# Optimization experiments

Measured on AMD Instinct MI355X. Metric: run time of the kernel, lower is better.

## Reference

```python
import jax, jax.numpy as jnp
import numpy as np

N_NODES = 100000
N_EDGES = 3200000
N_IN = 5
N_OUT = 16


def setup_inputs() -> dict:
    key = jax.random.key(0)
    k1, k2, k3, k4 = jax.random.split(key, 4)
    atom = jax.random.normal(k1, (N_NODES, N_IN), dtype=jnp.float32)
    edge_index = jax.random.randint(k2, (2, N_EDGES), 0, N_NODES, dtype=jnp.int64)
    # Linear(n_input=5, n_neural=16) parameters
    W = jax.random.normal(k3, (N_OUT, N_IN), dtype=jnp.float32) / np.sqrt(N_IN)
    b = jax.random.normal(k4, (N_OUT,), dtype=jnp.float32) * 0.01
    return {"atom": atom, "edge_index": edge_index, "W": W, "b": b}


def reference(atom, edge_index, W, b):
    n = atom.shape[0]
    # add_self_loops
    loops = jnp.arange(n, dtype=edge_index.dtype)
    row = jnp.concatenate([edge_index[0], loops])  # source nodes [E+N]
    col = jnp.concatenate([edge_index[1], loops])  # target nodes [E+N]
    # x = Linear(atom)
    x = atom @ W.T + b  # [N, n_out]
    # degree over target index (includes self loops -> deg >= 1)
    deg = jax.ops.segment_sum(jnp.ones_like(col, dtype=x.dtype), col, num_segments=n)
    dis = deg ** -0.5  # deg_inv_sqrt, finite since deg >= 1
    norm = dis[row] * dis[col]  # [E+N]
    # gather-scale-scatter: message = norm * x_j, aggr='add' at col
    msgs = norm[:, None] * x[row]  # [E+N, n_out]
    out = jax.ops.segment_sum(msgs, col, num_segments=n)  # [N, n_out]
    return jax.nn.relu(out)
```

## Files before the change

kernel.cpp:

```cpp
#include <hip/hip_runtime.h>

#define N_IN 5
#define N_OUT 16
#define NB 256
#define BN 400
#define CAP 14336
#define QSCALE 1024.0f
#define QBIAS 8192
#define BIN_MAGIC 10737419ull

__device__ __forceinline__ int bin_of(int c) {
    return (int)(((unsigned long long)(unsigned)c * BIN_MAGIC) >> 32);
}

__global__ void init_kernel(int* __restrict__ cursor) {
    if (threadIdx.x < NB) cursor[threadIdx.x] = threadIdx.x * CAP;
}

__global__ __launch_bounds__(1024) void partition_kernel(
        const int* __restrict__ row, const int* __restrict__ col,
        int e, int* __restrict__ eb, int* __restrict__ cursor) {
    __shared__ int hist[NB];
    __shared__ int base[NB];
    int e4 = e >> 2;
    int nchunk = (e4 + 1023) / 1024;
    const int4* rowv = (const int4*)row;
    const int4* colv = (const int4*)col;
    for (int ch = blockIdx.x; ch < nchunk; ch += gridDim.x) {
        int i = ch * 1024 + threadIdx.x;
        bool valid = i < e4;
        int rr[4], cc[4], bb[4], pr[4];
        if (valid) {
            int4 r4 = rowv[i];
            int4 c4 = colv[i];
            rr[0] = r4.x; rr[1] = r4.y; rr[2] = r4.z; rr[3] = r4.w;
            cc[0] = c4.x; cc[1] = c4.y; cc[2] = c4.z; cc[3] = c4.w;
        }
        if (threadIdx.x < NB) hist[threadIdx.x] = 0;
        __syncthreads();
        if (valid) {
#pragma unroll
            for (int j = 0; j < 4; ++j) {
                bb[j] = bin_of(cc[j]);
                pr[j] = atomicAdd(&hist[bb[j]], 1);
            }
        }
        __syncthreads();
        if (threadIdx.x < NB) {
            int h = hist[threadIdx.x];
            base[threadIdx.x] = h ? atomicAdd(&cursor[threadIdx.x], h) : 0;
        }
        __syncthreads();
        if (valid) {
#pragma unroll
            for (int j = 0; j < 4; ++j) {
                int p = base[bb[j]] + pr[j];
                if (p < (bb[j] + 1) * CAP)
                    eb[p] = ((cc[j] - bb[j] * BN) << 17) | rr[j];
            }
        }
        __syncthreads();
    }
    if (blockIdx.x == 0) {
        for (int i = (e4 << 2) + (int)threadIdx.x; i < e; i += (int)blockDim.x) {
            int c = col[i];
            int b = bin_of(c);
            int p = atomicAdd(&cursor[b], 1);
            if (p < (b + 1) * CAP) eb[p] = ((c - b * BN) << 17) | row[i];
        }
    }
}

__global__ __launch_bounds__(1024) void deg_quant_kernel(
        const int* __restrict__ eb, const int* __restrict__ cursor,
        const float* __restrict__ atom,
        ulonglong2* __restrict__ qdatom, unsigned short* __restrict__ deg16,
        int n) {
    __shared__ int hist[BN];
    int bin = blockIdx.x;
    if (threadIdx.x < BN) hist[threadIdx.x] = 0;
    __syncthreads();
    int s0 = bin * CAP;
    int cnt = min(max(cursor[bin] - s0, 0), CAP);
    const int4* ebv = (const int4*)(eb + s0);
    int cnt4 = cnt >> 2;
    for (int i = threadIdx.x; i < cnt4; i += 1024) {
        int4 v = ebv[i];
        atomicAdd(&hist[v.x >> 17], 1);
        atomicAdd(&hist[v.y >> 17], 1);
        atomicAdd(&hist[v.z >> 17], 1);
        atomicAdd(&hist[v.w >> 17], 1);
    }
    for (int i = (cnt4 << 2) + (int)threadIdx.x; i < cnt; i += 1024)
        atomicAdd(&hist[eb[s0 + i] >> 17], 1);
    __syncthreads();
    int l = threadIdx.x;
    if (l >= BN) return;
    int node = bin * BN + l;
    if (node >= n) return;
    int deg = hist[l];
    deg16[node] = (unsigned short)deg;
    float d = rsqrtf((float)(deg + 1));
    const float* ap = atom + (size_t)node * N_IN;
    unsigned long long f[6];
#pragma unroll
    for (int k = 0; k < 5; ++k) {
        int q = __float2int_rn(d * ap[k] * QSCALE);
        q = min(max(q, -8191), 8191);
        f[k] = (unsigned long long)(q + QBIAS);
    }
    f[5] = (unsigned long long)(__float2int_rn(d * QSCALE) + QBIAS);
    ulonglong2 v;
    v.x = f[0] | (f[1] << 21) | (f[2] << 42);
    v.y = f[3] | (f[4] << 21) | (f[5] << 42);
    qdatom[node] = v;
}

__global__ __launch_bounds__(1024) void accum_final(
        const int* __restrict__ eb, const int* __restrict__ cursor,
        const ulonglong2* __restrict__ qdatom,
        const unsigned short* __restrict__ deg16,
        const float* __restrict__ atom,
        const float* __restrict__ W, const float* __restrict__ bias,
        float* __restrict__ out, int n) {
    __shared__ unsigned long long accA[BN];
    __shared__ unsigned long long accB[BN];
    int bin = blockIdx.x;
    if (threadIdx.x < BN) { accA[threadIdx.x] = 0ull; accB[threadIdx.x] = 0ull; }
    __syncthreads();
    int s0 = bin * CAP;
    int cnt = min(max(cursor[bin] - s0, 0), CAP);
    const int4* ebv = (const int4*)(eb + s0);
    int cnt4 = cnt >> 2;
    for (int i = threadIdx.x; i < cnt4; i += 1024) {
        int4 v = ebv[i];
        ulonglong2 q0 = qdatom[v.x & 0x1FFFF];
        ulonglong2 q1 = qdatom[v.y & 0x1FFFF];
        ulonglong2 q2 = qdatom[v.z & 0x1FFFF];
        ulonglong2 q3 = qdatom[v.w & 0x1FFFF];
        atomicAdd(&accA[v.x >> 17], q0.x);
        atomicAdd(&accB[v.x >> 17], q0.y);
        atomicAdd(&accA[v.y >> 17], q1.x);
        atomicAdd(&accB[v.y >> 17], q1.y);
        atomicAdd(&accA[v.z >> 17], q2.x);
        atomicAdd(&accB[v.z >> 17], q2.y);
        atomicAdd(&accA[v.w >> 17], q3.x);
        atomicAdd(&accB[v.w >> 17], q3.y);
    }
    for (int i = (cnt4 << 2) + (int)threadIdx.x; i < cnt; i += 1024) {
        int v = eb[s0 + i];
        ulonglong2 q = qdatom[v & 0x1FFFF];
        atomicAdd(&accA[v >> 17], q.x);
        atomicAdd(&accB[v >> 17], q.y);
    }
    __syncthreads();
    int l = threadIdx.x;
    if (l >= BN) return;
    int node = bin * BN + l;
    if (node >= n) return;
    unsigned long long SA = accA[l], SB = accB[l];
    int deg = deg16[node];
    int db = deg * QBIAS;
    const float inv = 1.0f / QSCALE;
    float s[6];
    s[0] = (float)((int)((SA      ) & 0x1FFFFF) - db) * inv;
    s[1] = (float)((int)((SA >> 21) & 0x1FFFFF) - db) * inv;
    s[2] = (float)((int)((SA >> 42) & 0x1FFFFF) - db) * inv;
    s[3] = (float)((int)((SB      ) & 0x1FFFFF) - db) * inv;
    s[4] = (float)((int)((SB >> 21) & 0x1FFFFF) - db) * inv;
    s[5] = (float)((int)((SB >> 42) & 0x1FFFFF) - db) * inv;
    float d = rsqrtf((float)(deg + 1));
    const float* ap = atom + (size_t)node * N_IN;
    float t5[5];
#pragma unroll
    for (int k = 0; k < 5; ++k) t5[k] = d * (s[k] + d * ap[k]);
    float t1 = d * (s[5] + d);
    float ov[N_OUT];
#pragma unroll
    for (int o = 0; o < N_OUT; ++o) {
        float a = bias[o] * t1;
#pragma unroll
        for (int k = 0; k < 5; ++k) a = fmaf(W[o * N_IN + k], t5[k], a);
        ov[o] = fmaxf(a, 0.0f);
    }
    float4* op = (float4*)(out + (size_t)node * N_OUT);
#pragma unroll
    for (int q = 0; q < 4; ++q)
        op[q] = make_float4(ov[4 * q], ov[4 * q + 1], ov[4 * q + 2], ov[4 * q + 3]);
}

extern "C" void kernel_launch(void* const* d_in, const int* in_sizes, int n_in,
                              void* d_out, int out_size, void* d_ws, size_t ws_size,
                              hipStream_t stream) {
    const float* atom = (const float*)d_in[0];
    const int*   eidx = (const int*)d_in[1];
    const float* W    = (const float*)d_in[2];
    const float* b    = (const float*)d_in[3];
    float* out = (float*)d_out;

    int n = in_sizes[0] / N_IN;
    int e = in_sizes[1] / 2;
    const int* row = eidx;
    const int* col = eidx + e;

    auto align256 = [](size_t v) { return (v + 255) & ~(size_t)255; };
    char* w = (char*)d_ws;
    int*            cursor = (int*)w;            w += align256(NB * 4);
    int*            eb     = (int*)w;            w += align256((size_t)NB * CAP * 4);
    ulonglong2*     qdatom = (ulonglong2*)w;     w += align256((size_t)NB * BN * 16);
    unsigned short* deg16  = (unsigned short*)w;

    init_kernel<<<1, NB, 0, stream>>>(cursor);
    partition_kernel<<<256, 1024, 0, stream>>>(row, col, e, eb, cursor);
    deg_quant_kernel<<<NB, 1024, 0, stream>>>(eb, cursor, atom, qdatom, deg16, n);
    accum_final<<<NB, 1024, 0, stream>>>(eb, cursor, qdatom, deg16, atom, W, b, out, n);
}
```

Baseline: 126.2 us.

## Fuse degree/quantize and accumulate kernels via cooperative grid sync with register-held edges

Merges the degree-histogram/quantization kernel and the accumulate/finalize kernel into one cooperative kernel. The kernel loads each bin's edges into registers once, builds the degree histogram, writes the quantized scaled features, does a grid-wide sync, then gathers and accumulates from the same registers. This drops the second read of the edge buckets, the deg16 buffer and one launch. The cursor is now a per-bin offset cleared by a memset instead of an init kernel. It depends on cooperative launch with 256 blocks of 1024 threads all being resident, and it holds at most 4096 int4 per bin in registers, which matches CAP.

```diff
diff --git a/kernel.cpp b/kernel.cpp
--- a/kernel.cpp
+++ b/kernel.cpp
@@ -1,4 +1,7 @@
 #include <hip/hip_runtime.h>
+#include <hip/hip_cooperative_groups.h>
+
+namespace cg = cooperative_groups;
 
 #define N_IN 5
 #define N_OUT 16
@@ -11,10 +14,6 @@
 
 __device__ __forceinline__ int bin_of(int c) {
     return (int)(((unsigned long long)(unsigned)c * BIN_MAGIC) >> 32);
-}
-
-__global__ void init_kernel(int* __restrict__ cursor) {
-    if (threadIdx.x < NB) cursor[threadIdx.x] = threadIdx.x * CAP;
 }
 
 __global__ __launch_bounds__(1024) void partition_kernel(
@@ -54,9 +53,9 @@
         if (valid) {
 #pragma unroll
             for (int j = 0; j < 4; ++j) {
-                int p = base[bb[j]] + pr[j];
-                if (p < (bb[j] + 1) * CAP)
-                    eb[p] = ((cc[j] - bb[j] * BN) << 17) | rr[j];
+                int o = base[bb[j]] + pr[j];
+                if (o < CAP)
+                    eb[bb[j] * CAP + o] = ((cc[j] - bb[j] * BN) << 17) | rr[j];
             }
         }
         __syncthreads();
@@ -65,102 +64,104 @@
         for (int i = (e4 << 2) + (int)threadIdx.x; i < e; i += (int)blockDim.x) {
             int c = col[i];
             int b = bin_of(c);
-            int p = atomicAdd(&cursor[b], 1);
-            if (p < (b + 1) * CAP) eb[p] = ((c - b * BN) << 17) | row[i];
-        }
-    }
-}
-
-__global__ __launch_bounds__(1024) void deg_quant_kernel(
+            int o = atomicAdd(&cursor[b], 1);
+            if (o < CAP) eb[b * CAP + o] = ((c - b * BN) << 17) | row[i];
+        }
+    }
+}
+
+__global__ __launch_bounds__(1024) void fused_deg_accum(
         const int* __restrict__ eb, const int* __restrict__ cursor,
         const float* __restrict__ atom,
-        ulonglong2* __restrict__ qdatom, unsigned short* __restrict__ deg16,
-        int n) {
-    __shared__ int hist[BN];
-    int bin = blockIdx.x;
-    if (threadIdx.x < BN) hist[threadIdx.x] = 0;
-    __syncthreads();
-    int s0 = bin * CAP;
-    int cnt = min(max(cursor[bin] - s0, 0), CAP);
-    const int4* ebv = (const int4*)(eb + s0);
-    int cnt4 = cnt >> 2;
-    for (int i = threadIdx.x; i < cnt4; i += 1024) {
-        int4 v = ebv[i];
-        atomicAdd(&hist[v.x >> 17], 1);
-        atomicAdd(&hist[v.y >> 17], 1);
-        atomicAdd(&hist[v.z >> 17], 1);
-        atomicAdd(&hist[v.w >> 17], 1);
-    }
-    for (int i = (cnt4 << 2) + (int)threadIdx.x; i < cnt; i += 1024)
-        atomicAdd(&hist[eb[s0 + i] >> 17], 1);
-    __syncthreads();
-    int l = threadIdx.x;
-    if (l >= BN) return;
-    int node = bin * BN + l;
-    if (node >= n) return;
-    int deg = hist[l];
-    deg16[node] = (unsigned short)deg;
-    float d = rsqrtf((float)(deg + 1));
-    const float* ap = atom + (size_t)node * N_IN;
-    unsigned long long f[6];
-#pragma unroll
-    for (int k = 0; k < 5; ++k) {
-        int q = __float2int_rn(d * ap[k] * QSCALE);
-        q = min(max(q, -8191), 8191);
-        f[k] = (unsigned long long)(q + QBIAS);
-    }
-    f[5] = (unsigned long long)(__float2int_rn(d * QSCALE) + QBIAS);
-    ulonglong2 v;
-    v.x = f[0] | (f[1] << 21) | (f[2] << 42);
-    v.y = f[3] | (f[4] << 21) | (f[5] << 42);
-    qdatom[node] = v;
-}
-
-__global__ __launch_bounds__(1024) void accum_final(
-        const int* __restrict__ eb, const int* __restrict__ cursor,
-        const ulonglong2* __restrict__ qdatom,
-        const unsigned short* __restrict__ deg16,
-        const float* __restrict__ atom,
+        ulonglong2* __restrict__ qdatom,
         const float* __restrict__ W, const float* __restrict__ bias,
         float* __restrict__ out, int n) {
+    __shared__ int hist[BN];
     __shared__ unsigned long long accA[BN];
     __shared__ unsigned long long accB[BN];
-    int bin = blockIdx.x;
-    if (threadIdx.x < BN) { accA[threadIdx.x] = 0ull; accB[threadIdx.x] = 0ull; }
+    cg::grid_group grid = cg::this_grid();
+    const int bin = blockIdx.x;
+    const int tid = threadIdx.x;
+    if (tid < BN) { hist[tid] = 0; accA[tid] = 0ull; accB[tid] = 0ull; }
     __syncthreads();
-    int s0 = bin * CAP;
-    int cnt = min(max(cursor[bin] - s0, 0), CAP);
+
+    const int s0 = bin * CAP;
+    const int cnt = min(max(cursor[bin], 0), CAP);
+    const int cnt4 = cnt >> 2;
     const int4* ebv = (const int4*)(eb + s0);
-    int cnt4 = cnt >> 2;
-    for (int i = threadIdx.x; i < cnt4; i += 1024) {
-        int4 v = ebv[i];
-        ulonglong2 q0 = qdatom[v.x & 0x1FFFF];
-        ulonglong2 q1 = qdatom[v.y & 0x1FFFF];
-        ulonglong2 q2 = qdatom[v.z & 0x1FFFF];
-        ulonglong2 q3 = qdatom[v.w & 0x1FFFF];
-        atomicAdd(&accA[v.x >> 17], q0.x);
-        atomicAdd(&accB[v.x >> 17], q0.y);
-        atomicAdd(&accA[v.y >> 17], q1.x);
-        atomicAdd(&accB[v.y >> 17], q1.y);
-        atomicAdd(&accA[v.z >> 17], q2.x);
-        atomicAdd(&accB[v.z >> 17], q2.y);
-        atomicAdd(&accA[v.w >> 17], q3.x);
-        atomicAdd(&accB[v.w >> 17], q3.y);
-    }
-    for (int i = (cnt4 << 2) + (int)threadIdx.x; i < cnt; i += 1024) {
-        int v = eb[s0 + i];
-        ulonglong2 q = qdatom[v & 0x1FFFF];
-        atomicAdd(&accA[v >> 17], q.x);
-        atomicAdd(&accB[v >> 17], q.y);
-    }
+
+    int4 e0, e1, e2, e3;
+    const bool v0 = tid          < cnt4;
+    const bool v1 = tid + 1024   < cnt4;
+    const bool v2 = tid + 2048   < cnt4;
+    const bool v3 = tid + 3072   < cnt4;
+    if (v0) e0 = ebv[tid];
+    if (v1) e1 = ebv[tid + 1024];
+    if (v2) e2 = ebv[tid + 2048];
+    if (v3) e3 = ebv[tid + 3072];
+    int tl = -1;
+    if (tid < (cnt & 3)) tl = eb[s0 + (cnt4 << 2) + tid];
+
+#define H4(E) { atomicAdd(&hist[(E).x >> 17], 1); atomicAdd(&hist[(E).y >> 17], 1); \
+                atomicAdd(&hist[(E).z >> 17], 1); atomicAdd(&hist[(E).w >> 17], 1); }
+    if (v0) H4(e0);
+    if (v1) H4(e1);
+    if (v2) H4(e2);
+    if (v3) H4(e3);
+#undef H4
+    if (tl >= 0) atomicAdd(&hist[tl >> 17], 1);
     __syncthreads();
-    int l = threadIdx.x;
-    if (l >= BN) return;
-    int node = bin * BN + l;
-    if (node >= n) return;
-    unsigned long long SA = accA[l], SB = accB[l];
-    int deg = deg16[node];
-    int db = deg * QBIAS;
+
+    int mydeg = 0;
+    float a0 = 0.f, a1 = 0.f, a2 = 0.f, a3 = 0.f, a4 = 0.f;
+    const int node = bin * BN + tid;
+    const bool own = (tid < BN) && (node < n);
+    if (own) {
+        mydeg = hist[tid];
+        float d = rsqrtf((float)(mydeg + 1));
+        const float* ap = atom + (size_t)node * N_IN;
+        a0 = ap[0]; a1 = ap[1]; a2 = ap[2]; a3 = ap[3]; a4 = ap[4];
+        unsigned long long f[6];
+        float av[5] = {a0, a1, a2, a3, a4};
+#pragma unroll
+        for (int k = 0; k < 5; ++k) {
+            int q = __float2int_rn(d * av[k] * QSCALE);
+            q = min(max(q, -8191), 8191);
+            f[k] = (unsigned long long)(q + QBIAS);
+        }
+        f[5] = (unsigned long long)(__float2int_rn(d * QSCALE) + QBIAS);
+        ulonglong2 v;
+        v.x = f[0] | (f[1] << 21) | (f[2] << 42);
+        v.y = f[3] | (f[4] << 21) | (f[5] << 42);
+        qdatom[node] = v;
+    }
+    __threadfence();
+    grid.sync();
+
+#define A4(E) { \
+        ulonglong2 q0 = qdatom[(E).x & 0x1FFFF]; \
+        ulonglong2 q1 = qdatom[(E).y & 0x1FFFF]; \
+        ulonglong2 q2 = qdatom[(E).z & 0x1FFFF]; \
+        ulonglong2 q3 = qdatom[(E).w & 0x1FFFF]; \
+        atomicAdd(&accA[(E).x >> 17], q0.x); atomicAdd(&accB[(E).x >> 17], q0.y); \
+        atomicAdd(&accA[(E).y >> 17], q1.x); atomicAdd(&accB[(E).y >> 17], q1.y); \
+        atomicAdd(&accA[(E).z >> 17], q2.x); atomicAdd(&accB[(E).z >> 17], q2.y); \
+        atomicAdd(&accA[(E).w >> 17], q3.x); atomicAdd(&accB[(E).w >> 17], q3.y); }
+    if (v0) A4(e0);
+    if (v1) A4(e1);
+    if (v2) A4(e2);
+    if (v3) A4(e3);
+#undef A4
+    if (tl >= 0) {
+        ulonglong2 q = qdatom[tl & 0x1FFFF];
+        atomicAdd(&accA[tl >> 17], q.x);
+        atomicAdd(&accB[tl >> 17], q.y);
+    }
+    __syncthreads();
+
+    if (!own) return;
+    unsigned long long SA = accA[tid], SB = accB[tid];
+    int db = mydeg * QBIAS;
     const float inv = 1.0f / QSCALE;
     float s[6];
     s[0] = (float)((int)((SA      ) & 0x1FFFFF) - db) * inv;
@@ -169,11 +170,11 @@
     s[3] = (float)((int)((SB      ) & 0x1FFFFF) - db) * inv;
     s[4] = (float)((int)((SB >> 21) & 0x1FFFFF) - db) * inv;
     s[5] = (float)((int)((SB >> 42) & 0x1FFFFF) - db) * inv;
-    float d = rsqrtf((float)(deg + 1));
-    const float* ap = atom + (size_t)node * N_IN;
+    float d = rsqrtf((float)(mydeg + 1));
     float t5[5];
-#pragma unroll
-    for (int k = 0; k < 5; ++k) t5[k] = d * (s[k] + d * ap[k]);
+    float av[5] = {a0, a1, a2, a3, a4};
+#pragma unroll
+    for (int k = 0; k < 5; ++k) t5[k] = d * (s[k] + d * av[k]);
     float t1 = d * (s[5] + d);
     float ov[N_OUT];
 #pragma unroll
@@ -205,13 +206,18 @@
 
     auto align256 = [](size_t v) { return (v + 255) & ~(size_t)255; };
     char* w = (char*)d_ws;
-    int*            cursor = (int*)w;            w += align256(NB * 4);
-    int*            eb     = (int*)w;            w += align256((size_t)NB * CAP * 4);
-    ulonglong2*     qdatom = (ulonglong2*)w;     w += align256((size_t)NB * BN * 16);
-    unsigned short* deg16  = (unsigned short*)w;
-
-    init_kernel<<<1, NB, 0, stream>>>(cursor);
+    int*        cursor = (int*)w;        w += align256(NB * 4);
+    int*        eb     = (int*)w;        w += align256((size_t)NB * CAP * 4);
+    ulonglong2* qdatom = (ulonglong2*)w;
+
+    hipMemsetAsync(cursor, 0, NB * sizeof(int), stream);
     partition_kernel<<<256, 1024, 0, stream>>>(row, col, e, eb, cursor);
-    deg_quant_kernel<<<NB, 1024, 0, stream>>>(eb, cursor, atom, qdatom, deg16, n);
-    accum_final<<<NB, 1024, 0, stream>>>(eb, cursor, qdatom, deg16, atom, W, b, out, n);
-}
+
+    const int* eb_c = eb;
+    const int* cursor_c = cursor;
+    void* kargs[] = { (void*)&eb_c, (void*)&cursor_c, (void*)&atom,
+                      (void*)&qdatom, (void*)&W, (void*)&b,
+                      (void*)&out, (void*)&n };
+    hipLaunchCooperativeKernel((void*)fused_deg_accum, dim3(NB), dim3(1024),
+                               kargs, 0, stream);
+}
```

Measured after the change: 230.3 us. 82.5% more time.

## Compute node degrees with global atomics during partition, drop degree-histogram pass

Applied to the files above, without the earlier changes.

Moves the in-degree count into the partition kernel as per-edge global atomicAdds on a zeroed degree array, so the separate kernel that re-read every bin's edges to histogram degrees is replaced by a light per-node quantization kernel. The init kernel is replaced by a memset that zeroes both the cursors (now relative offsets) and the degree array. This removes one full pass over the 3.2M binned edges but adds 3.2M random global atomics to the partition phase, which may contend or add latency.

```diff
diff --git a/kernel.cpp b/kernel.cpp
--- a/kernel.cpp
+++ b/kernel.cpp
@@ -13,13 +13,10 @@
     return (int)(((unsigned long long)(unsigned)c * BIN_MAGIC) >> 32);
 }
 
-__global__ void init_kernel(int* __restrict__ cursor) {
-    if (threadIdx.x < NB) cursor[threadIdx.x] = threadIdx.x * CAP;
-}
-
 __global__ __launch_bounds__(1024) void partition_kernel(
         const int* __restrict__ row, const int* __restrict__ col,
-        int e, int* __restrict__ eb, int* __restrict__ cursor) {
+        int e, int* __restrict__ eb, int* __restrict__ cursor,
+        int* __restrict__ deg) {
     __shared__ int hist[NB];
     __shared__ int base[NB];
     int e4 = e >> 2;
@@ -43,6 +40,7 @@
             for (int j = 0; j < 4; ++j) {
                 bb[j] = bin_of(cc[j]);
                 pr[j] = atomicAdd(&hist[bb[j]], 1);
+                atomicAdd(&deg[cc[j]], 1);
             }
         }
         __syncthreads();
@@ -54,9 +52,9 @@
         if (valid) {
 #pragma unroll
             for (int j = 0; j < 4; ++j) {
-                int p = base[bb[j]] + pr[j];
-                if (p < (bb[j] + 1) * CAP)
-                    eb[p] = ((cc[j] - bb[j] * BN) << 17) | rr[j];
+                int o = base[bb[j]] + pr[j];
+                if (o < CAP)
+                    eb[bb[j] * CAP + o] = ((cc[j] - bb[j] * BN) << 17) | rr[j];
             }
         }
         __syncthreads();
@@ -65,42 +63,19 @@
         for (int i = (e4 << 2) + (int)threadIdx.x; i < e; i += (int)blockDim.x) {
             int c = col[i];
             int b = bin_of(c);
-            int p = atomicAdd(&cursor[b], 1);
-            if (p < (b + 1) * CAP) eb[p] = ((c - b * BN) << 17) | row[i];
+            int o = atomicAdd(&cursor[b], 1);
+            atomicAdd(&deg[c], 1);
+            if (o < CAP) eb[b * CAP + o] = ((c - b * BN) << 17) | row[i];
         }
     }
 }
 
-__global__ __launch_bounds__(1024) void deg_quant_kernel(
-        const int* __restrict__ eb, const int* __restrict__ cursor,
-        const float* __restrict__ atom,
-        ulonglong2* __restrict__ qdatom, unsigned short* __restrict__ deg16,
-        int n) {
-    __shared__ int hist[BN];
-    int bin = blockIdx.x;
-    if (threadIdx.x < BN) hist[threadIdx.x] = 0;
-    __syncthreads();
-    int s0 = bin * CAP;
-    int cnt = min(max(cursor[bin] - s0, 0), CAP);
-    const int4* ebv = (const int4*)(eb + s0);
-    int cnt4 = cnt >> 2;
-    for (int i = threadIdx.x; i < cnt4; i += 1024) {
-        int4 v = ebv[i];
-        atomicAdd(&hist[v.x >> 17], 1);
-        atomicAdd(&hist[v.y >> 17], 1);
-        atomicAdd(&hist[v.z >> 17], 1);
-        atomicAdd(&hist[v.w >> 17], 1);
-    }
-    for (int i = (cnt4 << 2) + (int)threadIdx.x; i < cnt; i += 1024)
-        atomicAdd(&hist[eb[s0 + i] >> 17], 1);
-    __syncthreads();
-    int l = threadIdx.x;
-    if (l >= BN) return;
-    int node = bin * BN + l;
+__global__ __launch_bounds__(256) void quant_kernel(
+        const int* __restrict__ deg, const float* __restrict__ atom,
+        ulonglong2* __restrict__ qdatom, int n) {
+    int node = blockIdx.x * 256 + threadIdx.x;
     if (node >= n) return;
-    int deg = hist[l];
-    deg16[node] = (unsigned short)deg;
-    float d = rsqrtf((float)(deg + 1));
+    float d = rsqrtf((float)(deg[node] + 1));
     const float* ap = atom + (size_t)node * N_IN;
     unsigned long long f[6];
 #pragma unroll
@@ -119,7 +94,7 @@
 __global__ __launch_bounds__(1024) void accum_final(
         const int* __restrict__ eb, const int* __restrict__ cursor,
         const ulonglong2* __restrict__ qdatom,
-        const unsigned short* __restrict__ deg16,
+        const int* __restrict__ deg,
         const float* __restrict__ atom,
         const float* __restrict__ W, const float* __restrict__ bias,
         float* __restrict__ out, int n) {
@@ -129,7 +104,7 @@
     if (threadIdx.x < BN) { accA[threadIdx.x] = 0ull; accB[threadIdx.x] = 0ull; }
     __syncthreads();
     int s0 = bin * CAP;
-    int cnt = min(max(cursor[bin] - s0, 0), CAP);
+    int cnt = min(max(cursor[bin], 0), CAP);
     const int4* ebv = (const int4*)(eb + s0);
     int cnt4 = cnt >> 2;
     for (int i = threadIdx.x; i < cnt4; i += 1024) {
@@ -159,8 +134,8 @@
     int node = bin * BN + l;
     if (node >= n) return;
     unsigned long long SA = accA[l], SB = accB[l];
-    int deg = deg16[node];
-    int db = deg * QBIAS;
+    int dg = deg[node];
+    int db = dg * QBIAS;
     const float inv = 1.0f / QSCALE;
     float s[6];
     s[0] = (float)((int)((SA      ) & 0x1FFFFF) - db) * inv;
@@ -169,7 +144,7 @@
     s[3] = (float)((int)((SB      ) & 0x1FFFFF) - db) * inv;
     s[4] = (float)((int)((SB >> 21) & 0x1FFFFF) - db) * inv;
     s[5] = (float)((int)((SB >> 42) & 0x1FFFFF) - db) * inv;
-    float d = rsqrtf((float)(deg + 1));
+    float d = rsqrtf((float)(dg + 1));
     const float* ap = atom + (size_t)node * N_IN;
     float t5[5];
 #pragma unroll
@@ -205,13 +180,14 @@
 
     auto align256 = [](size_t v) { return (v + 255) & ~(size_t)255; };
     char* w = (char*)d_ws;
-    int*            cursor = (int*)w;            w += align256(NB * 4);
-    int*            eb     = (int*)w;            w += align256((size_t)NB * CAP * 4);
-    ulonglong2*     qdatom = (ulonglong2*)w;     w += align256((size_t)NB * BN * 16);
-    unsigned short* deg16  = (unsigned short*)w;
+    int*        cursor = (int*)w;     w += align256(NB * 4);
+    int*        deg    = (int*)w;     w += align256((size_t)NB * BN * 4);
+    int*        eb     = (int*)w;     w += align256((size_t)NB * CAP * 4);
+    ulonglong2* qdatom = (ulonglong2*)w;
 
-    init_kernel<<<1, NB, 0, stream>>>(cursor);
-    partition_kernel<<<256, 1024, 0, stream>>>(row, col, e, eb, cursor);
-    deg_quant_kernel<<<NB, 1024, 0, stream>>>(eb, cursor, atom, qdatom, deg16, n);
-    accum_final<<<NB, 1024, 0, stream>>>(eb, cursor, qdatom, deg16, atom, W, b, out, n);
+    size_t zbytes = align256(NB * 4) + align256((size_t)NB * BN * 4);
+    hipMemsetAsync(cursor, 0, zbytes, stream);
+    partition_kernel<<<256, 1024, 0, stream>>>(row, col, e, eb, cursor, deg);
+    quant_kernel<<<(100000 + 255) / 256, 256, 0, stream>>>(deg, atom, qdatom, 100000 > 0 ? ((int)((in_sizes[0]) / N_IN)) : 0);
+    accum_final<<<NB, 1024, 0, stream>>>(eb, cursor, qdatom, deg, atom, W, b, out, n);
 }
```

Result: slower. 243.0 us (+92.6%).

## Launch one partition block per 2048-vector chunk and replace init kernel with memset

Applied to the files above, without the earlier changes.

The partition kernel stops looping over chunks in a fixed grid of 256 blocks. It now launches one block per 8192 edges, and each thread handles two int4 groups with a single histogram/cursor-reservation round. The cursor becomes a per-bin relative count initialised with hipMemsetAsync instead of a separate init kernel, and the consumers read counts directly. The aim is to remove the per-chunk barriers and serial loop, expose more parallelism and drop a kernel launch. The cost is many more blocks each doing one global atomic per bin.

```diff
diff --git a/kernel.cpp b/kernel.cpp
--- a/kernel.cpp
+++ b/kernel.cpp
@@ -13,60 +13,77 @@
     return (int)(((unsigned long long)(unsigned)c * BIN_MAGIC) >> 32);
 }
 
-__global__ void init_kernel(int* __restrict__ cursor) {
-    if (threadIdx.x < NB) cursor[threadIdx.x] = threadIdx.x * CAP;
-}
-
 __global__ __launch_bounds__(1024) void partition_kernel(
         const int* __restrict__ row, const int* __restrict__ col,
         int e, int* __restrict__ eb, int* __restrict__ cursor) {
     __shared__ int hist[NB];
     __shared__ int base[NB];
-    int e4 = e >> 2;
-    int nchunk = (e4 + 1023) / 1024;
+    const int tid = threadIdx.x;
+    const int e4 = e >> 2;
+    const int i0 = blockIdx.x * 2048 + tid;
+    const int i1 = i0 + 1024;
+    const bool valid0 = i0 < e4;
+    const bool valid1 = i1 < e4;
     const int4* rowv = (const int4*)row;
     const int4* colv = (const int4*)col;
-    for (int ch = blockIdx.x; ch < nchunk; ch += gridDim.x) {
-        int i = ch * 1024 + threadIdx.x;
-        bool valid = i < e4;
-        int rr[4], cc[4], bb[4], pr[4];
-        if (valid) {
-            int4 r4 = rowv[i];
-            int4 c4 = colv[i];
-            rr[0] = r4.x; rr[1] = r4.y; rr[2] = r4.z; rr[3] = r4.w;
-            cc[0] = c4.x; cc[1] = c4.y; cc[2] = c4.z; cc[3] = c4.w;
-        }
-        if (threadIdx.x < NB) hist[threadIdx.x] = 0;
-        __syncthreads();
-        if (valid) {
-#pragma unroll
-            for (int j = 0; j < 4; ++j) {
-                bb[j] = bin_of(cc[j]);
-                pr[j] = atomicAdd(&hist[bb[j]], 1);
-            }
-        }
-        __syncthreads();
-        if (threadIdx.x < NB) {
-            int h = hist[threadIdx.x];
-            base[threadIdx.x] = h ? atomicAdd(&cursor[threadIdx.x], h) : 0;
-        }
-        __syncthreads();
-        if (valid) {
-#pragma unroll
-            for (int j = 0; j < 4; ++j) {
-                int p = base[bb[j]] + pr[j];
-                if (p < (bb[j] + 1) * CAP)
-                    eb[p] = ((cc[j] - bb[j] * BN) << 17) | rr[j];
-            }
-        }
-        __syncthreads();
+    int rr0[4], cc0[4], bb0[4], pr0[4];
+    int rr1[4], cc1[4], bb1[4], pr1[4];
+    if (valid0) {
+        int4 r4 = rowv[i0];
+        int4 c4 = colv[i0];
+        rr0[0] = r4.x; rr0[1] = r4.y; rr0[2] = r4.z; rr0[3] = r4.w;
+        cc0[0] = c4.x; cc0[1] = c4.y; cc0[2] = c4.z; cc0[3] = c4.w;
+    }
+    if (valid1) {
+        int4 r4 = rowv[i1];
+        int4 c4 = colv[i1];
+        rr1[0] = r4.x; rr1[1] = r4.y; rr1[2] = r4.z; rr1[3] = r4.w;
+        cc1[0] = c4.x; cc1[1] = c4.y; cc1[2] = c4.z; cc1[3] = c4.w;
+    }
+    if (tid < NB) hist[tid] = 0;
+    __syncthreads();
+    if (valid0) {
+#pragma unroll
+        for (int j = 0; j < 4; ++j) {
+            bb0[j] = bin_of(cc0[j]);
+            pr0[j] = atomicAdd(&hist[bb0[j]], 1);
+        }
+    }
+    if (valid1) {
+#pragma unroll
+        for (int j = 0; j < 4; ++j) {
+            bb1[j] = bin_of(cc1[j]);
+            pr1[j] = atomicAdd(&hist[bb1[j]], 1);
+        }
+    }
+    __syncthreads();
+    if (tid < NB) {
+        int h = hist[tid];
+        base[tid] = h ? atomicAdd(&cursor[tid], h) : 0;
+    }
+    __syncthreads();
+    if (valid0) {
+#pragma unroll
+        for (int j = 0; j < 4; ++j) {
+            int p = base[bb0[j]] + pr0[j];
+            if (p < CAP)
+                eb[bb0[j] * CAP + p] = ((cc0[j] - bb0[j] * BN) << 17) | rr0[j];
+        }
+    }
+    if (valid1) {
+#pragma unroll
+        for (int j = 0; j < 4; ++j) {
+            int p = base[bb1[j]] + pr1[j];
+            if (p < CAP)
+                eb[bb1[j] * CAP + p] = ((cc1[j] - bb1[j] * BN) << 17) | rr1[j];
+        }
     }
     if (blockIdx.x == 0) {
-        for (int i = (e4 << 2) + (int)threadIdx.x; i < e; i += (int)blockDim.x) {
-            int c = col[i];
+        for (int k = (e4 << 2) + tid; k < e; k += 1024) {
+            int c = col[k];
             int b = bin_of(c);
-            int p = atomicAdd(&cursor[b], 1);
-            if (p < (b + 1) * CAP) eb[p] = ((c - b * BN) << 17) | row[i];
+            int o = atomicAdd(&cursor[b], 1);
+            if (o < CAP) eb[b * CAP + o] = ((c - b * BN) << 17) | row[k];
         }
     }
 }
@@ -81,7 +98,7 @@
     if (threadIdx.x < BN) hist[threadIdx.x] = 0;
     __syncthreads();
     int s0 = bin * CAP;
-    int cnt = min(max(cursor[bin] - s0, 0), CAP);
+    int cnt = min(max(cursor[bin], 0), CAP);
     const int4* ebv = (const int4*)(eb + s0);
     int cnt4 = cnt >> 2;
     for (int i = threadIdx.x; i < cnt4; i += 1024) {
@@ -129,7 +146,7 @@
     if (threadIdx.x < BN) { accA[threadIdx.x] = 0ull; accB[threadIdx.x] = 0ull; }
     __syncthreads();
     int s0 = bin * CAP;
-    int cnt = min(max(cursor[bin] - s0, 0), CAP);
+    int cnt = min(max(cursor[bin], 0), CAP);
     const int4* ebv = (const int4*)(eb + s0);
     int cnt4 = cnt >> 2;
     for (int i = threadIdx.x; i < cnt4; i += 1024) {
@@ -210,8 +227,11 @@
     ulonglong2*     qdatom = (ulonglong2*)w;     w += align256((size_t)NB * BN * 16);
     unsigned short* deg16  = (unsigned short*)w;
 
-    init_kernel<<<1, NB, 0, stream>>>(cursor);
-    partition_kernel<<<256, 1024, 0, stream>>>(row, col, e, eb, cursor);
+    int nchunk = ((e >> 2) + 2047) / 2048;
+    if (nchunk < 1) nchunk = 1;
+
+    hipMemsetAsync(cursor, 0, NB * sizeof(int), stream);
+    partition_kernel<<<nchunk, 1024, 0, stream>>>(row, col, e, eb, cursor);
     deg_quant_kernel<<<NB, 1024, 0, stream>>>(eb, cursor, atom, qdatom, deg16, n);
     accum_final<<<NB, 1024, 0, stream>>>(eb, cursor, qdatom, deg16, atom, W, b, out, n);
 }
```

New measurement: 123.9 us. No clear change (-1.8%).
